# Performance work log

Hardware: AMD Instinct MI355X
Metric: run time of the kernel (lower is better)

Reference implementation:

```python
import jax, jax.numpy as jnp
import numpy as np

EPS = 1e-6


def setup_inputs() -> dict:
    key = jax.random.key(0)
    k1, k2, k3, k4, k5, k6 = jax.random.split(key, 6)
    B, S = 32, 1024
    H, W = 32, 32            # max_n_patches_h/w
    C, P = 3, 16             # channels, patch_res
    D = C * P * P            # 768
    P2 = P * P               # 256
    patches = jax.random.normal(k1, (B, S, D), dtype=jnp.float32)
    pos_h = jax.random.randint(k2, (B, S), 0, H)
    pos_w = jax.random.randint(k3, (B, S), 0, W)
    key_pad_mask = jax.random.bernoulli(k4, 0.1, (B, S))  # True where padding
    n = jnp.zeros((H, W), dtype=jnp.float32)
    mean = 0.1 * jax.random.normal(k5, (H, W, P2), dtype=jnp.float32)
    m2 = jax.random.uniform(k6, (H, W, P2), dtype=jnp.float32)
    return {"patches": patches, "pos_h": pos_h, "pos_w": pos_w,
            "key_pad_mask": key_pad_mask, "n": n, "mean": mean, "m2": m2}


def reference(patches, pos_h, pos_w, key_pad_mask, n, mean, m2):
    """PatchNorm.forward in training mode (Welford update + normalize).

    Masked (padded) positions contribute 0 to the scatter sums and are
    written back as zeros, matching the torch boolean-mask gather/scatter.
    """
    H, W, P2 = mean.shape
    B, S, D = patches.shape
    C = D // P2
    HW = H * W

    x = patches.reshape(B * S, C, P2)                    # (N, c, p^2)
    pf = (pos_h * W + pos_w).reshape(-1)                 # (N,) flat grid index
    w = (~key_pad_mask).reshape(-1).astype(patches.dtype)  # 1.0 on valid tokens

    # --- Welford online update (torch scatter_add semantics w/ duplicates) ---
    counts = jax.ops.segment_sum(w, pf, num_segments=HW)
    n_new = n + counts.reshape(H, W)

    mean_flat = mean.reshape(HW, P2)
    delta = (x - mean_flat[pf][:, None, :]).mean(axis=1) * w[:, None]  # (N, p^2)
    n_g = jnp.maximum(n_new.reshape(HW)[pf], 1.0)
    mean_new_flat = mean_flat + jax.ops.segment_sum(delta / n_g[:, None], pf, num_segments=HW)
    mean_new = mean_new_flat.reshape(H, W, P2)

    delta2 = (x - mean_new_flat[pf][:, None, :]).mean(axis=1) * w[:, None]
    m2_new = m2 + jax.ops.segment_sum(delta * delta2, pf, num_segments=HW).reshape(H, W, P2)

    # --- var / std (var := 1 where n < 2) ---
    var = jnp.where((n_new < 2.0)[..., None], 1.0,
                    m2_new / jnp.maximum(n_new, 1.0)[..., None])
    std = jnp.sqrt(var)

    # --- normalize with gathered per-position stats, zero out padding ---
    mg = mean_new.reshape(HW, P2)[pf][:, None, :]        # (N, 1, p^2)
    sg = std.reshape(HW, P2)[pf][:, None, :]
    out = (x - mg) / (sg + EPS) * w[:, None, None]
    return out.reshape(B, S, D)
```

## Files before the change

### kernel.cpp

```cpp
#include <hip/hip_runtime.h>
#include <math.h>


#define EPSF 1e-6f

static constexpr int W_GRID  = 32;
static constexpr int P2      = 256;
static constexpr int P4      = 64;
static constexpr int D4      = 192;
static constexpr int HW      = 1024;
static constexpr int NTOK    = 32768;
static constexpr int LISTCAP = 96;

__global__ void k_pf(const int* __restrict__ pos_h,
                     const int* __restrict__ pos_w,
                     const int* __restrict__ mask,
                     unsigned short* __restrict__ pf16) {
    int i = blockIdx.x * blockDim.x + threadIdx.x;
    if (i >= NTOK) return;
    const int valid = (mask[i] == 0);
    pf16[i] = valid ? (unsigned short)(pos_h[i] * W_GRID + pos_w[i])
                    : (unsigned short)0xFFFF;
}

__global__ void __launch_bounds__(256, 4)
k_moments(const float4* __restrict__ patches4,
          const unsigned short* __restrict__ pf16,
          const float* __restrict__ n_old,
          const float* __restrict__ mean_old,
          const float* __restrict__ m2_old,
          float* __restrict__ mean_new,
          float* __restrict__ inv_std) {
    const int g    = blockIdx.x;
    const int tid  = threadIdx.x;
    const int wave = tid >> 6;
    const int lane = tid & 63;

    __shared__ int    list[LISTCAP];
    __shared__ int    s_cnt;
    __shared__ float4 l14[4][64];
    __shared__ float4 l24[4][64];

    if (tid == 0) s_cnt = 0;

    const int4* pp = (const int4*)pf16;
    int4 v[16];
#pragma unroll
    for (int it = 0; it < 16; ++it) v[it] = pp[it * 256 + tid];
    __syncthreads();

#pragma unroll
    for (int it = 0; it < 16; ++it) {
        const int base = (it * 256 + tid) * 8;
#pragma unroll
        for (int k = 0; k < 4; ++k) {
            const int word = (&v[it].x)[k];
            const int g0 = word & 0xFFFF;
            const int g1 = (word >> 16) & 0xFFFF;
            if (g0 == g) { int s = atomicAdd(&s_cnt, 1); if (s < LISTCAP) list[s] = base + 2 * k; }
            if (g1 == g) { int s = atomicAdd(&s_cnt, 1); if (s < LISTCAP) list[s] = base + 2 * k + 1; }
        }
    }
    __syncthreads();
    const int c = min(s_cnt, LISTCAP);

    float4 s1 = make_float4(0.f, 0.f, 0.f, 0.f);
    float4 s2 = make_float4(0.f, 0.f, 0.f, 0.f);
    for (int k = wave; k < c; k += 16) {
        int   idx[4];
        float wf[4];
#pragma unroll
        for (int j = 0; j < 4; ++j) {
            const int  kk  = k + 4 * j;
            const bool val = (kk < c);
            wf[j]  = val ? 1.0f : 0.0f;
            idx[j] = list[val ? kk : k];
        }
        float4 A[4], B[4], Dd[4];
#pragma unroll
        for (int j = 0; j < 4; ++j) {
            const float4* tp = patches4 + (size_t)idx[j] * D4;
            A[j]  = tp[lane];
            B[j]  = tp[lane + P4];
            Dd[j] = tp[lane + 2 * P4];
        }
#pragma unroll
        for (int j = 0; j < 4; ++j) {
            const float f = (1.0f / 3.0f) * wf[j];
            float4 xb;
            xb.x = (A[j].x + B[j].x + Dd[j].x) * f;
            xb.y = (A[j].y + B[j].y + Dd[j].y) * f;
            xb.z = (A[j].z + B[j].z + Dd[j].z) * f;
            xb.w = (A[j].w + B[j].w + Dd[j].w) * f;
            s1.x += xb.x; s1.y += xb.y; s1.z += xb.z; s1.w += xb.w;
            s2.x += xb.x * xb.x; s2.y += xb.y * xb.y;
            s2.z += xb.z * xb.z; s2.w += xb.w * xb.w;
        }
    }

    l14[wave][lane] = s1;
    l24[wave][lane] = s2;
    __syncthreads();

    const float* l1f = (const float*)l14;
    const float* l2f = (const float*)l24;
    const float S1 = l1f[tid] + l1f[256 + tid] + l1f[512 + tid] + l1f[768 + tid];
    const float S2 = l2f[tid] + l2f[256 + tid] + l2f[512 + tid] + l2f[768 + tid];

    const float cnt = (float)c;
    const float nn  = n_old[g] + cnt;
    const float ng  = fmaxf(nn, 1.0f);
    const int   j   = g * P2 + tid;
    const float mo  = mean_old[j];
    const float mn  = mo + (S1 - cnt * mo) / ng;
    const float m2n = m2_old[j] + (S2 - (mo + mn) * S1 + cnt * mo * mn);
    const float var = (nn < 2.0f) ? 1.0f : (m2n / ng);
    mean_new[j] = mn;
    inv_std[j]  = 1.0f / (sqrtf(var) + EPSF);
}

static constexpr int CPB = 1536;
__global__ void __launch_bounds__(256, 4)
k_norm(const float4* __restrict__ patches4,
       const unsigned short* __restrict__ pf16,
       const float4* __restrict__ mn4,
       const float4* __restrict__ is4,
       float4* __restrict__ out4) {
    const int b    = blockIdx.x;
    const int tid  = threadIdx.x;
    const int cbase = b * CPB;
    const int tok0  = b * 8;

    __shared__ unsigned short s_gg[8];
    if (tid < 8) s_gg[tid] = pf16[tok0 + tid];

    float4 x[6];
#pragma unroll
    for (int j = 0; j < 6; ++j) x[j] = patches4[cbase + j * 256 + tid];
    __syncthreads();

    int   gx[6], pidx[6];
    float wv[6];
#pragma unroll
    for (int j = 0; j < 6; ++j) {
        const int local = j * 256 + tid;
        const int lt    = local / 192;
        pidx[j] = (local - lt * 192) & 63;
        const unsigned short gg = s_gg[lt];
        wv[j] = (gg != 0xFFFF) ? 1.0f : 0.0f;
        gx[j] = (gg != 0xFFFF) ? (int)gg : 0;
    }

    float4 m[6], s[6];
#pragma unroll
    for (int j = 0; j < 6; ++j) {
        m[j] = mn4[gx[j] * P4 + pidx[j]];
        s[j] = is4[gx[j] * P4 + pidx[j]];
    }
#pragma unroll
    for (int j = 0; j < 6; ++j) {
        float4 o;
        o.x = (x[j].x - m[j].x) * s[j].x * wv[j];
        o.y = (x[j].y - m[j].y) * s[j].y * wv[j];
        o.z = (x[j].z - m[j].z) * s[j].z * wv[j];
        o.w = (x[j].w - m[j].w) * s[j].w * wv[j];
        out4[cbase + j * 256 + tid] = o;
    }
}

extern "C" void kernel_launch(void* const* d_in, const int* in_sizes, int n_in,
                              void* d_out, int out_size, void* d_ws, size_t ws_size,
                              hipStream_t stream) {
    const float4* patches4 = (const float4*)d_in[0];
    const int*    pos_h    = (const int*)d_in[1];
    const int*    pos_w    = (const int*)d_in[2];
    const int*    mask     = (const int*)d_in[3];
    const float*  n_old    = (const float*)d_in[4];
    const float*  mean     = (const float*)d_in[5];
    const float*  m2       = (const float*)d_in[6];
    float4* out4 = (float4*)d_out;

    unsigned short* pf16 = (unsigned short*)d_ws;
    float* mean_new = (float*)(pf16 + NTOK);
    float* inv_std  = mean_new + (size_t)HW * P2;

    k_pf<<<NTOK / 256, 256, 0, stream>>>(pos_h, pos_w, mask, pf16);
    k_moments<<<HW, 256, 0, stream>>>(patches4, pf16, n_old, mean, m2,
                                      mean_new, inv_std);
    k_norm<<<(NTOK * D4) / CPB, 256, 0, stream>>>(patches4, pf16,
                                                  (const float4*)mean_new,
                                                  (const float4*)inv_std, out4);
}
```

Before: 64.84 us.

## Precompute channel-mean xbar in a coalesced prep pass before per-cell stats

Replaces the index kernel with a prep kernel that, besides computing flat grid indices, streams all patches once in token order and writes the channel-averaged vector (xbar) to workspace. The stats kernel then gathers 1 KB xbar rows instead of 3 KB patch rows per token, cutting its scattered-gather traffic. In exchange it adds a full extra read of the patches plus a write and re-read of a 32 MB buffer, and it falls back to the old path when the workspace is too small. Launch-bound occupancy hints were also loosened.

```diff
diff --git a/kernel.cpp b/kernel.cpp
--- a/kernel.cpp
+++ b/kernel.cpp
@@ -11,26 +11,50 @@
 static constexpr int HW      = 1024;
 static constexpr int NTOK    = 32768;
 static constexpr int LISTCAP = 96;
-
-__global__ void k_pf(const int* __restrict__ pos_h,
-                     const int* __restrict__ pos_w,
-                     const int* __restrict__ mask,
-                     unsigned short* __restrict__ pf16) {
-    int i = blockIdx.x * blockDim.x + threadIdx.x;
-    if (i >= NTOK) return;
-    const int valid = (mask[i] == 0);
-    pf16[i] = valid ? (unsigned short)(pos_h[i] * W_GRID + pos_w[i])
-                    : (unsigned short)0xFFFF;
-}
-
-__global__ void __launch_bounds__(256, 4)
-k_moments(const float4* __restrict__ patches4,
-          const unsigned short* __restrict__ pf16,
-          const float* __restrict__ n_old,
-          const float* __restrict__ mean_old,
-          const float* __restrict__ m2_old,
-          float* __restrict__ mean_new,
-          float* __restrict__ inv_std) {
+static constexpr int CPB     = 1536;
+
+__global__ void __launch_bounds__(256)
+k_prep(const float4* __restrict__ patches4,
+       const int* __restrict__ pos_h,
+       const int* __restrict__ pos_w,
+       const int* __restrict__ mask,
+       unsigned short* __restrict__ pf16,
+       float4* __restrict__ xbar4,
+       int do_xbar) {
+    const int tid  = threadIdx.x;
+    const int wave = tid >> 6;
+    const int lane = tid & 63;
+    const int i    = blockIdx.x * 4 + wave;
+
+    if (lane == 0) {
+        const int valid = (mask[i] == 0);
+        pf16[i] = valid ? (unsigned short)(pos_h[i] * W_GRID + pos_w[i])
+                        : (unsigned short)0xFFFF;
+    }
+    if (do_xbar) {
+        const float4* tp = patches4 + (size_t)i * D4 + lane;
+        const float4 a = tp[0];
+        const float4 b = tp[P4];
+        const float4 d = tp[2 * P4];
+        float4 xb;
+        xb.x = (a.x + b.x + d.x) * (1.0f / 3.0f);
+        xb.y = (a.y + b.y + d.y) * (1.0f / 3.0f);
+        xb.z = (a.z + b.z + d.z) * (1.0f / 3.0f);
+        xb.w = (a.w + b.w + d.w) * (1.0f / 3.0f);
+        xbar4[(size_t)i * P4 + lane] = xb;
+    }
+}
+
+__global__ void __launch_bounds__(256)
+k_stats(const float4* __restrict__ patches4,
+        const float4* __restrict__ xbar4,
+        const unsigned short* __restrict__ pf16,
+        const float* __restrict__ n_old,
+        const float* __restrict__ mean_old,
+        const float* __restrict__ m2_old,
+        float* __restrict__ mean_new,
+        float* __restrict__ inv_std,
+        int use_xbar) {
     const int g    = blockIdx.x;
     const int tid  = threadIdx.x;
     const int wave = tid >> 6;
@@ -66,35 +90,63 @@
 
     float4 s1 = make_float4(0.f, 0.f, 0.f, 0.f);
     float4 s2 = make_float4(0.f, 0.f, 0.f, 0.f);
-    for (int k = wave; k < c; k += 16) {
-        int   idx[4];
-        float wf[4];
-#pragma unroll
-        for (int j = 0; j < 4; ++j) {
-            const int  kk  = k + 4 * j;
-            const bool val = (kk < c);
-            wf[j]  = val ? 1.0f : 0.0f;
-            idx[j] = list[val ? kk : k];
+
+    if (use_xbar) {
+        for (int k = wave; k < c; k += 16) {
+            int   idx[4];
+            float wf[4];
+#pragma unroll
+            for (int j = 0; j < 4; ++j) {
+                const int  kk  = k + 4 * j;
+                const bool val = (kk < c);
+                wf[j]  = val ? 1.0f : 0.0f;
+                idx[j] = list[val ? kk : k];
+            }
+            float4 X[4];
+#pragma unroll
+            for (int j = 0; j < 4; ++j)
+                X[j] = xbar4[(size_t)idx[j] * P4 + lane];
+#pragma unroll
+            for (int j = 0; j < 4; ++j) {
+                float4 xb;
+                xb.x = X[j].x * wf[j];  xb.y = X[j].y * wf[j];
+                xb.z = X[j].z * wf[j];  xb.w = X[j].w * wf[j];
+                s1.x += xb.x; s1.y += xb.y; s1.z += xb.z; s1.w += xb.w;
+                s2.x += xb.x * xb.x; s2.y += xb.y * xb.y;
+                s2.z += xb.z * xb.z; s2.w += xb.w * xb.w;
+            }
         }
-        float4 A[4], B[4], Dd[4];
-#pragma unroll
-        for (int j = 0; j < 4; ++j) {
-            const float4* tp = patches4 + (size_t)idx[j] * D4;
-            A[j]  = tp[lane];
-            B[j]  = tp[lane + P4];
-            Dd[j] = tp[lane + 2 * P4];
-        }
-#pragma unroll
-        for (int j = 0; j < 4; ++j) {
-            const float f = (1.0f / 3.0f) * wf[j];
-            float4 xb;
-            xb.x = (A[j].x + B[j].x + Dd[j].x) * f;
-            xb.y = (A[j].y + B[j].y + Dd[j].y) * f;
-            xb.z = (A[j].z + B[j].z + Dd[j].z) * f;
-            xb.w = (A[j].w + B[j].w + Dd[j].w) * f;
-            s1.x += xb.x; s1.y += xb.y; s1.z += xb.z; s1.w += xb.w;
-            s2.x += xb.x * xb.x; s2.y += xb.y * xb.y;
-            s2.z += xb.z * xb.z; s2.w += xb.w * xb.w;
+    } else {
+        for (int k = wave; k < c; k += 16) {
+            int   idx[4];
+            float wf[4];
+#pragma unroll
+            for (int j = 0; j < 4; ++j) {
+                const int  kk  = k + 4 * j;
+                const bool val = (kk < c);
+                wf[j]  = val ? 1.0f : 0.0f;
+                idx[j] = list[val ? kk : k];
+            }
+            float4 A[4], B[4], Dd[4];
+#pragma unroll
+            for (int j = 0; j < 4; ++j) {
+                const float4* tp = patches4 + (size_t)idx[j] * D4 + lane;
+                A[j]  = tp[0];
+                B[j]  = tp[P4];
+                Dd[j] = tp[2 * P4];
+            }
+#pragma unroll
+            for (int j = 0; j < 4; ++j) {
+                const float f = (1.0f / 3.0f) * wf[j];
+                float4 xb;
+                xb.x = (A[j].x + B[j].x + Dd[j].x) * f;
+                xb.y = (A[j].y + B[j].y + Dd[j].y) * f;
+                xb.z = (A[j].z + B[j].z + Dd[j].z) * f;
+                xb.w = (A[j].w + B[j].w + Dd[j].w) * f;
+                s1.x += xb.x; s1.y += xb.y; s1.z += xb.z; s1.w += xb.w;
+                s2.x += xb.x * xb.x; s2.y += xb.y * xb.y;
+                s2.z += xb.z * xb.z; s2.w += xb.w * xb.w;
+            }
         }
     }
 
@@ -119,15 +171,14 @@
     inv_std[j]  = 1.0f / (sqrtf(var) + EPSF);
 }
 
-static constexpr int CPB = 1536;
-__global__ void __launch_bounds__(256, 4)
+__global__ void __launch_bounds__(256)
 k_norm(const float4* __restrict__ patches4,
        const unsigned short* __restrict__ pf16,
        const float4* __restrict__ mn4,
        const float4* __restrict__ is4,
        float4* __restrict__ out4) {
-    const int b    = blockIdx.x;
-    const int tid  = threadIdx.x;
+    const int b     = blockIdx.x;
+    const int tid   = threadIdx.x;
     const int cbase = b * CPB;
     const int tok0  = b * 8;
 
@@ -183,10 +234,16 @@
     unsigned short* pf16 = (unsigned short*)d_ws;
     float* mean_new = (float*)(pf16 + NTOK);
     float* inv_std  = mean_new + (size_t)HW * P2;
-
-    k_pf<<<NTOK / 256, 256, 0, stream>>>(pos_h, pos_w, mask, pf16);
-    k_moments<<<HW, 256, 0, stream>>>(patches4, pf16, n_old, mean, m2,
-                                      mean_new, inv_std);
+    float* xbar     = inv_std + (size_t)HW * P2;
+
+    const size_t need = (size_t)NTOK * 2 + (size_t)2 * HW * P2 * 4
+                      + (size_t)NTOK * P2 * 4;
+    const int use_xbar = (ws_size >= need) ? 1 : 0;
+
+    k_prep<<<NTOK / 4, 256, 0, stream>>>(patches4, pos_h, pos_w, mask,
+                                         pf16, (float4*)xbar, use_xbar);
+    k_stats<<<HW, 256, 0, stream>>>(patches4, (const float4*)xbar, pf16,
+                                    n_old, mean, m2, mean_new, inv_std, use_xbar);
     k_norm<<<(NTOK * D4) / CPB, 256, 0, stream>>>(patches4, pf16,
                                                   (const float4*)mean_new,
                                                   (const float4*)inv_std, out4);
```

Result: slower. 71.68 us (+10.6%).

## Precompute channel-mean in bf16 in a prep pass, stage stats in LDS for normalize

Applied to the files above, without the earlier changes.

Fuses the grid-index computation with a new pass that reads every patch once, averages the three channels, and stores the result as bf16 in the output buffer used as scratch. The stats kernel then gathers these compact 512-byte rows instead of the full 3 KB fp32 patches. The normalize kernel now loads each block's 8 per-position mean and inv-std rows into shared memory once rather than gathering them per element. This adds a full streaming pass over the patches and a bf16 write, and it lowers the precision of the moments, which risks accuracy.

```diff
diff --git a/kernel.cpp b/kernel.cpp
--- a/kernel.cpp
+++ b/kernel.cpp
@@ -11,26 +11,54 @@
 static constexpr int HW      = 1024;
 static constexpr int NTOK    = 32768;
 static constexpr int LISTCAP = 96;
-
-__global__ void k_pf(const int* __restrict__ pos_h,
-                     const int* __restrict__ pos_w,
-                     const int* __restrict__ mask,
-                     unsigned short* __restrict__ pf16) {
-    int i = blockIdx.x * blockDim.x + threadIdx.x;
-    if (i >= NTOK) return;
-    const int valid = (mask[i] == 0);
-    pf16[i] = valid ? (unsigned short)(pos_h[i] * W_GRID + pos_w[i])
-                    : (unsigned short)0xFFFF;
-}
-
-__global__ void __launch_bounds__(256, 4)
-k_moments(const float4* __restrict__ patches4,
-          const unsigned short* __restrict__ pf16,
-          const float* __restrict__ n_old,
-          const float* __restrict__ mean_old,
-          const float* __restrict__ m2_old,
-          float* __restrict__ mean_new,
-          float* __restrict__ inv_std) {
+static constexpr int CPB     = 1536;
+
+__device__ __forceinline__ unsigned short f2bf(float f) {
+    unsigned int u = __float_as_uint(f);
+    u += 0x7FFFu + ((u >> 16) & 1u);
+    return (unsigned short)(u >> 16);
+}
+__device__ __forceinline__ float bf2f(unsigned short h) {
+    return __uint_as_float(((unsigned int)h) << 16);
+}
+
+__global__ void __launch_bounds__(256)
+k_prep(const float4* __restrict__ patches4,
+       const int* __restrict__ pos_h,
+       const int* __restrict__ pos_w,
+       const int* __restrict__ mask,
+       unsigned short* __restrict__ pf16,
+       ushort4* __restrict__ xbarh) {
+    const int tid  = threadIdx.x;
+    const int wave = tid >> 6;
+    const int lane = tid & 63;
+    const int i    = blockIdx.x * 4 + wave;
+
+    if (lane == 0) {
+        const int valid = (mask[i] == 0);
+        pf16[i] = valid ? (unsigned short)(pos_h[i] * W_GRID + pos_w[i])
+                        : (unsigned short)0xFFFF;
+    }
+    const float4* tp = patches4 + (size_t)i * D4 + lane;
+    const float4 a = tp[0];
+    const float4 b = tp[P4];
+    const float4 d = tp[2 * P4];
+    ushort4 h;
+    h.x = f2bf((a.x + b.x + d.x) * (1.0f / 3.0f));
+    h.y = f2bf((a.y + b.y + d.y) * (1.0f / 3.0f));
+    h.z = f2bf((a.z + b.z + d.z) * (1.0f / 3.0f));
+    h.w = f2bf((a.w + b.w + d.w) * (1.0f / 3.0f));
+    xbarh[(size_t)i * P4 + lane] = h;
+}
+
+__global__ void __launch_bounds__(256)
+k_stats(const ushort4* __restrict__ xbarh,
+        const unsigned short* __restrict__ pf16,
+        const float* __restrict__ n_old,
+        const float* __restrict__ mean_old,
+        const float* __restrict__ m2_old,
+        float* __restrict__ mean_new,
+        float* __restrict__ inv_std) {
     const int g    = blockIdx.x;
     const int tid  = threadIdx.x;
     const int wave = tid >> 6;
@@ -76,22 +104,17 @@
             wf[j]  = val ? 1.0f : 0.0f;
             idx[j] = list[val ? kk : k];
         }
-        float4 A[4], B[4], Dd[4];
+        ushort4 X[4];
+#pragma unroll
+        for (int j = 0; j < 4; ++j)
+            X[j] = xbarh[(size_t)idx[j] * P4 + lane];
 #pragma unroll
         for (int j = 0; j < 4; ++j) {
-            const float4* tp = patches4 + (size_t)idx[j] * D4;
-            A[j]  = tp[lane];
-            B[j]  = tp[lane + P4];
-            Dd[j] = tp[lane + 2 * P4];
-        }
-#pragma unroll
-        for (int j = 0; j < 4; ++j) {
-            const float f = (1.0f / 3.0f) * wf[j];
             float4 xb;
-            xb.x = (A[j].x + B[j].x + Dd[j].x) * f;
-            xb.y = (A[j].y + B[j].y + Dd[j].y) * f;
-            xb.z = (A[j].z + B[j].z + Dd[j].z) * f;
-            xb.w = (A[j].w + B[j].w + Dd[j].w) * f;
+            xb.x = bf2f(X[j].x) * wf[j];
+            xb.y = bf2f(X[j].y) * wf[j];
+            xb.z = bf2f(X[j].z) * wf[j];
+            xb.w = bf2f(X[j].w) * wf[j];
             s1.x += xb.x; s1.y += xb.y; s1.z += xb.z; s1.w += xb.w;
             s2.x += xb.x * xb.x; s2.y += xb.y * xb.y;
             s2.z += xb.z * xb.z; s2.w += xb.w * xb.w;
@@ -119,51 +142,53 @@
     inv_std[j]  = 1.0f / (sqrtf(var) + EPSF);
 }
 
-static constexpr int CPB = 1536;
-__global__ void __launch_bounds__(256, 4)
+__global__ void __launch_bounds__(256)
 k_norm(const float4* __restrict__ patches4,
        const unsigned short* __restrict__ pf16,
        const float4* __restrict__ mn4,
        const float4* __restrict__ is4,
        float4* __restrict__ out4) {
-    const int b    = blockIdx.x;
-    const int tid  = threadIdx.x;
+    const int b     = blockIdx.x;
+    const int tid   = threadIdx.x;
     const int cbase = b * CPB;
     const int tok0  = b * 8;
 
     __shared__ unsigned short s_gg[8];
+    __shared__ float4 mn_s[8][64];
+    __shared__ float4 is_s[8][64];
+
+    float4 x[6];
+#pragma unroll
+    for (int j = 0; j < 6; ++j) x[j] = patches4[cbase + j * 256 + tid];
+
     if (tid < 8) s_gg[tid] = pf16[tok0 + tid];
-
-    float4 x[6];
-#pragma unroll
-    for (int j = 0; j < 6; ++j) x[j] = patches4[cbase + j * 256 + tid];
-    __syncthreads();
-
-    int   gx[6], pidx[6];
-    float wv[6];
+    __syncthreads();
+
+    {
+        const int r  = tid >> 5;
+        const int q0 = tid & 31;
+        const unsigned short gg = s_gg[r];
+        const int gx = (gg != 0xFFFF) ? (int)gg : 0;
+        mn_s[r][q0]      = mn4[gx * P4 + q0];
+        mn_s[r][q0 + 32] = mn4[gx * P4 + q0 + 32];
+        is_s[r][q0]      = is4[gx * P4 + q0];
+        is_s[r][q0 + 32] = is4[gx * P4 + q0 + 32];
+    }
+    __syncthreads();
+
 #pragma unroll
     for (int j = 0; j < 6; ++j) {
         const int local = j * 256 + tid;
         const int lt    = local / 192;
-        pidx[j] = (local - lt * 192) & 63;
-        const unsigned short gg = s_gg[lt];
-        wv[j] = (gg != 0xFFFF) ? 1.0f : 0.0f;
-        gx[j] = (gg != 0xFFFF) ? (int)gg : 0;
-    }
-
-    float4 m[6], s[6];
-#pragma unroll
-    for (int j = 0; j < 6; ++j) {
-        m[j] = mn4[gx[j] * P4 + pidx[j]];
-        s[j] = is4[gx[j] * P4 + pidx[j]];
-    }
-#pragma unroll
-    for (int j = 0; j < 6; ++j) {
+        const int pp    = local & 63;
+        const float wv  = (s_gg[lt] != 0xFFFF) ? 1.0f : 0.0f;
+        const float4 m  = mn_s[lt][pp];
+        const float4 s  = is_s[lt][pp];
         float4 o;
-        o.x = (x[j].x - m[j].x) * s[j].x * wv[j];
-        o.y = (x[j].y - m[j].y) * s[j].y * wv[j];
-        o.z = (x[j].z - m[j].z) * s[j].z * wv[j];
-        o.w = (x[j].w - m[j].w) * s[j].w * wv[j];
+        o.x = (x[j].x - m.x) * s.x * wv;
+        o.y = (x[j].y - m.y) * s.y * wv;
+        o.z = (x[j].z - m.z) * s.z * wv;
+        o.w = (x[j].w - m.w) * s.w * wv;
         out4[cbase + j * 256 + tid] = o;
     }
 }
@@ -180,13 +205,16 @@
     const float*  m2       = (const float*)d_in[6];
     float4* out4 = (float4*)d_out;
 
+    ushort4* xbarh = (ushort4*)d_out;
+
     unsigned short* pf16 = (unsigned short*)d_ws;
     float* mean_new = (float*)(pf16 + NTOK);
     float* inv_std  = mean_new + (size_t)HW * P2;
 
-    k_pf<<<NTOK / 256, 256, 0, stream>>>(pos_h, pos_w, mask, pf16);
-    k_moments<<<HW, 256, 0, stream>>>(patches4, pf16, n_old, mean, m2,
-                                      mean_new, inv_std);
+    k_prep<<<NTOK / 4, 256, 0, stream>>>(patches4, pos_h, pos_w, mask,
+                                         pf16, xbarh);
+    k_stats<<<HW, 256, 0, stream>>>((const ushort4*)xbarh, pf16,
+                                    n_old, mean, m2, mean_new, inv_std);
     k_norm<<<(NTOK * D4) / CPB, 256, 0, stream>>>(patches4, pf16,
                                                   (const float4*)mean_new,
                                                   (const float4*)inv_std, out4);
```

After: 68.42 us. 1.06x slower.
